# Optimization experiments

Measured on AMD Instinct MI355X. Metric: run time of the kernel, lower is better.

The kernel has to match this reference:

```python
import jax, jax.numpy as jnp
import numpy as np
from functools import partial


@partial(jax.custom_vjp, nondiff_argnums=(1,))
def binarize1d(x, upper):
    return jnp.round(jnp.clip(x, 0.0, upper))

def _b1_fwd(x, upper):
    return jnp.round(jnp.clip(x, 0.0, upper)), x

def _b1_bwd(upper, x, g):
    # torch Binarize.backward for 1-D input: zero grad outside [0, upper]
    return (jnp.where((x < 0.0) | (x > upper), 0.0, g),)

binarize1d.defvjp(_b1_fwd, _b1_bwd)


def binarize2d(x, upper):
    # torch Binarize.backward for >=2-D input passes grad through unchanged -> STE
    return x + jax.lax.stop_gradient(jnp.round(jnp.clip(x, 0.0, upper)) - x)


def _perm_matrices(wc, wr, C, R):
    b = binarize1d(wc, float(C - 1))  # [C] selected row index per column
    # identity_column[i,j] = i  ->  col[i,j] = 1 iff i == b[j]
    col = binarize2d(1.0 - jnp.abs(jnp.arange(C, dtype=wc.dtype)[:, None] - b[None, :]), 1.0)
    r = binarize1d(wr, float(R - 1))  # [R] selected column index per row
    # identity_row[i,j] = j  ->  row[i,j] = 1 iff j == r[i]
    row = binarize2d(1.0 - jnp.abs(jnp.arange(R, dtype=wr.dtype)[None, :] - r[:, None]), 1.0)
    return col, row, b, r


def _fix_duplicates(sel, n):
    # sel: int32 [n]. Reassign every non-first occurrence of a value to an unused
    # slot. Deterministic stand-in for the original list + random.shuffle + pop():
    # unused slots are consumed in descending order (ascending list, pop from end).
    i = jnp.arange(n)
    eq = (sel[None, :] == sel[:, None]) & (i[:, None] < i[None, :])
    dup = eq.any(axis=0)  # dup[j]: sel[j] already seen at some earlier index
    counts = jnp.zeros((n,), jnp.int32).at[sel].add(1)
    empty_desc = jnp.sort(jnp.where(counts == 0, i, -1))[::-1]
    rank = jnp.cumsum(dup.astype(jnp.int32)) - 1
    return jnp.where(dup, empty_desc[rank], sel), dup


def _forward(x, weight_column, weight_row):
    C = weight_column.shape[0]
    R = weight_row.shape[0]
    # __update_rearrange_matrix__ : build selection indices from current weights
    _, _, b, r = _perm_matrices(weight_column, weight_row, C, R)
    bi = jax.lax.stop_gradient(b).astype(jnp.int32)
    ri = jax.lax.stop_gradient(r).astype(jnp.int32)
    # __constraint_rearrange_matrix__ : in-place .data rewrite of colliding entries
    new_b, dup_c = _fix_duplicates(bi, C)
    new_r, dup_r = _fix_duplicates(ri, R)
    wc = weight_column + jax.lax.stop_gradient(
        jnp.where(dup_c, new_b.astype(weight_column.dtype), weight_column) - weight_column)
    wr = weight_row + jax.lax.stop_gradient(
        jnp.where(dup_r, new_r.astype(weight_row.dtype), weight_row) - weight_row)
    # final __update_rearrange_matrix__ with the constrained weights
    col_mat, row_mat, _, _ = _perm_matrices(wc, wr, C, R)
    out = jnp.matmul(x, col_mat)    # [B, R, C] : column permutation
    out = jnp.matmul(row_mat, out)  # [B, R, C] : row permutation
    return out


def setup_inputs():
    key = jax.random.key(0)
    k1, k2, k3 = jax.random.split(key, 3)
    B, R, C = 16, 1024, 2048
    x = jax.random.normal(k1, (B, R, C), dtype=jnp.float32)
    weight_column = jax.random.uniform(k2, (C,), dtype=jnp.float32) * C  # uniform(0, C) as in reset_parameters
    weight_row = jax.random.uniform(k3, (R,), dtype=jnp.float32) * R
    return {"x": x, "weight_column": weight_column, "weight_row": weight_row}


def reference(x, weight_column, weight_row):
    return _forward(x, weight_column, weight_row)
```

## Files before the change

### kernel.cpp

```cpp
#include <hip/hip_runtime.h>

#define MAXN 2048

__global__ void build_map_kernel(const float* __restrict__ wc, const float* __restrict__ wr,
                                 int C, int R,
                                 int* __restrict__ colmap, int* __restrict__ rowmap) {
    const float* w;
    int n;
    int* outmap;
    if (blockIdx.x == 0) { w = wc; n = C; outmap = colmap; }
    else                 { w = wr; n = R; outmap = rowmap; }

    __shared__ int sel[MAXN];
    __shared__ int first[MAXN];
    __shared__ int emptyslot[MAXN];
    __shared__ int dts[256], ets[256];

    const int t = threadIdx.x;
    const int base = t * 8;
    const float upper = (float)(n - 1);

    for (int k = 0; k < 8; k++) {
        int idx = base + k;
        if (idx < n) {
            float v = w[idx];
            v = fminf(fmaxf(v, 0.0f), upper);
            sel[idx]   = (int)rintf(v);
            first[idx] = 0x7fffffff;
        }
    }
    __syncthreads();
    for (int k = 0; k < 8; k++) {
        int idx = base + k;
        if (idx < n) atomicMin(&first[sel[idx]], idx);
    }
    __syncthreads();

    int dflag[8], eflag[8];
    int dsum = 0, esum = 0;
    for (int k = 0; k < 8; k++) {
        int idx = base + k;
        if (idx < n) {
            dflag[k] = (first[sel[idx]] != idx) ? 1 : 0;
            eflag[k] = (first[idx] == 0x7fffffff) ? 1 : 0;
        } else { dflag[k] = 0; eflag[k] = 0; }
        dsum += dflag[k]; esum += eflag[k];
    }

    dts[t] = dsum; ets[t] = esum;
    __syncthreads();
    for (int off = 1; off < 256; off <<= 1) {
        int dv = 0, ev = 0;
        if (t >= off) { dv = dts[t - off]; ev = ets[t - off]; }
        __syncthreads();
        dts[t] += dv; ets[t] += ev;
        __syncthreads();
    }
    const int dexc = dts[t] - dsum;
    const int eexc = ets[t] - esum;
    const int E    = ets[255];

    int erun = eexc;
    for (int k = 0; k < 8; k++) {
        int idx = base + k;
        if (idx < n && eflag[k]) emptyslot[E - 1 - erun] = idx;
        erun += eflag[k];
    }
    __syncthreads();

    int drun = dexc;
    for (int k = 0; k < 8; k++) {
        int idx = base + k;
        if (idx < n) outmap[idx] = dflag[k] ? emptyslot[drun] : sel[idx];
        drun += dflag[k];
    }
}

__global__ void gather_kernel(const float* __restrict__ x,
                              const int* __restrict__ rowmap,
                              const int* __restrict__ colmap,
                              float* __restrict__ out,
                              int R, int C) {
    __shared__ float lds[MAXN];
    const int blk = blockIdx.x;
    const int b = blk / R;
    const int i = blk - b * R;
    const int sr = rowmap[i];

    const float4* src4 = (const float4*)(x + ((size_t)b * R + sr) * (size_t)C);
    float4*       dst4 = (float4*)(out + ((size_t)b * R + i) * (size_t)C);
    const int4*  cmap4 = (const int4*)colmap;

    const int t = threadIdx.x;
    const int n4 = C >> 2;

    for (int k = t; k < n4; k += 256) {
        ((float4*)lds)[k] = src4[k];
    }
    __syncthreads();
    for (int k = t; k < n4; k += 256) {
        int4 c = cmap4[k];
        float4 v;
        v.x = lds[c.x]; v.y = lds[c.y]; v.z = lds[c.z]; v.w = lds[c.w];
        dst4[k] = v;
    }
}

extern "C" void kernel_launch(void* const* d_in, const int* in_sizes, int n_in,
                              void* d_out, int out_size, void* d_ws, size_t ws_size,
                              hipStream_t stream) {
    const float* x  = (const float*)d_in[0];
    const float* wc = (const float*)d_in[1];
    const float* wr = (const float*)d_in[2];
    const int C = in_sizes[1];
    const int R = in_sizes[2];
    const int B = in_sizes[0] / (R * C);

    int* colmap = (int*)d_ws;
    int* rowmap = colmap + C;

    build_map_kernel<<<2, 256, 0, stream>>>(wc, wr, C, R, colmap, rowmap);
    gather_kernel<<<B * R, 256, 0, stream>>>(x, rowmap, colmap, (float*)d_out, R, C);
}
```

Before: 238.4 us.

## Assign one row per wavefront in gather kernel, dropping block barrier

The gather kernel now processes four rows per block, one per 64-lane wavefront, each with its own LDS slice, so the block-wide __syncthreads between the load and gather phases is removed. Loops are unrolled and output writes use nontemporal stores to avoid polluting cache. The cost is 32KB of LDS per block, which may limit occupancy. The design also relies on a wavefront reading back only its own LDS writes without an explicit barrier.

```diff
diff --git a/kernel.cpp b/kernel.cpp
--- a/kernel.cpp
+++ b/kernel.cpp
@@ -1,6 +1,9 @@
 #include <hip/hip_runtime.h>
 
 #define MAXN 2048
+
+typedef float f4v __attribute__((ext_vector_type(4)));
+typedef int   i4v __attribute__((ext_vector_type(4)));
 
 __global__ void build_map_kernel(const float* __restrict__ wc, const float* __restrict__ wr,
                                  int C, int R,
@@ -76,33 +79,44 @@
     }
 }
 
-__global__ void gather_kernel(const float* __restrict__ x,
+__global__ __launch_bounds__(256) void gather_kernel(const float* __restrict__ x,
                               const int* __restrict__ rowmap,
                               const int* __restrict__ colmap,
                               float* __restrict__ out,
-                              int R, int C) {
-    __shared__ float lds[MAXN];
-    const int blk = blockIdx.x;
-    const int b = blk / R;
-    const int i = blk - b * R;
+                              int R, int C, int nrows) {
+    __shared__ float lds[4 * MAXN];
+    const int t    = threadIdx.x;
+    const int w    = t >> 6;
+    const int lane = t & 63;
+
+    const int r = (blockIdx.x << 2) + w;
+    if (r >= nrows) return;
+
+    const int b  = r / R;
+    const int i  = r - b * R;
     const int sr = rowmap[i];
 
-    const float4* src4 = (const float4*)(x + ((size_t)b * R + sr) * (size_t)C);
-    float4*       dst4 = (float4*)(out + ((size_t)b * R + i) * (size_t)C);
-    const int4*  cmap4 = (const int4*)colmap;
+    float*       my   = lds + w * MAXN;
+    f4v*         my4  = (f4v*)my;
+    const f4v*   src4 = (const f4v*)(x + ((size_t)b * R + sr) * (size_t)C);
+    f4v*         dst4 = (f4v*)(out + (size_t)r * (size_t)C);
+    const i4v*  cmap4 = (const i4v*)colmap;
+    const int    n4   = C >> 2;
 
-    const int t = threadIdx.x;
-    const int n4 = C >> 2;
+    #pragma unroll 8
+    for (int k = lane; k < n4; k += 64) {
+        my4[k] = src4[k];
+    }
 
-    for (int k = t; k < n4; k += 256) {
-        ((float4*)lds)[k] = src4[k];
-    }
-    __syncthreads();
-    for (int k = t; k < n4; k += 256) {
-        int4 c = cmap4[k];
-        float4 v;
-        v.x = lds[c.x]; v.y = lds[c.y]; v.z = lds[c.z]; v.w = lds[c.w];
-        dst4[k] = v;
+    #pragma unroll 8
+    for (int k = lane; k < n4; k += 64) {
+        i4v c = cmap4[k];
+        f4v v;
+        v.x = my[c.x];
+        v.y = my[c.y];
+        v.z = my[c.z];
+        v.w = my[c.w];
+        __builtin_nontemporal_store(v, dst4 + k);
     }
 }
 
@@ -120,5 +134,8 @@
     int* rowmap = colmap + C;
 
     build_map_kernel<<<2, 256, 0, stream>>>(wc, wr, C, R, colmap, rowmap);
-    gather_kernel<<<B * R, 256, 0, stream>>>(x, rowmap, colmap, (float*)d_out, R, C);
+
+    const int nrows = B * R;
+    gather_kernel<<<(nrows + 3) / 4, 256, 0, stream>>>(x, rowmap, colmap,
+                                                       (float*)d_out, R, C, nrows);
 }
```

New measurement: 240.8 us. No clear change (+1.0%).
